# Performance work log

Measured on AMD Instinct MI355X. Metric: run time of the kernel, lower is better.

Reference implementation:

```python
import jax, jax.numpy as jnp
import numpy as np

B, N, C = 8, 4096, 1024
ATT_DIM = 512
M = 64  # num_outputs


def setup_inputs() -> dict:
    key = jax.random.key(0)
    k_x, k_w, k_b, k_av = jax.random.split(key, 4)
    x = jax.random.normal(k_x, (B, N, C), dtype=jnp.float32)
    # nn.Linear(input_dim, attention_dim): weight (att, C), bias (att,)
    lim = 1.0 / np.sqrt(C)
    W = jax.random.uniform(k_w, (ATT_DIM, C), dtype=jnp.float32, minval=-lim, maxval=lim)
    b = jax.random.uniform(k_b, (ATT_DIM,), dtype=jnp.float32, minval=-lim, maxval=lim)
    # torch.rand -> uniform [0,1)
    attention_vectors = jax.random.uniform(k_av, (M, ATT_DIM), dtype=jnp.float32)
    return {"x": x, "W": W, "b": b, "attention_vectors": attention_vectors}


def reference(x, W, b, attention_vectors):
    # linear projection: (B,N,C) @ (C,att) + bias -> (B,N,att)
    scores = jnp.einsum('bnc,dc->bnd', x, W) + b
    # learned-query attention logits: (B,M,N)
    logits = jnp.einsum('bnd,md->bmn', scores, attention_vectors)
    weights = jax.nn.softmax(logits, axis=-1)
    # pool original features: (B,M,N) @ (B,N,C) -> (B,M,C)
    return jnp.einsum('bmn,bnc->bmc', weights, x)
```

## Files before the change

### kernel.cpp

```cpp
#include <hip/hip_runtime.h>
#include <hip/hip_bf16.h>

#define Bn 8
#define Nn 4096
#define Cn 1024
#define Dn 512
#define Mn 64

typedef __hip_bfloat16 bf16;
typedef __attribute__((ext_vector_type(8))) short short8;
typedef __attribute__((ext_vector_type(4))) short short4x;
typedef __attribute__((ext_vector_type(4))) float f32x4;

#define MFMA16(a, b, c) __builtin_amdgcn_mfma_f32_16x16x32_bf16((a), (b), (c), 0, 0, 0)

__device__ inline short bfbits(float f) {
  union { bf16 b; short s; } u;
  u.b = __float2bfloat16(f);
  return u.s;
}

__device__ inline short8 pack8(const float4& a, const float4& b) {
  short8 s;
  s[0] = bfbits(a.x); s[1] = bfbits(a.y); s[2] = bfbits(a.z); s[3] = bfbits(a.w);
  s[4] = bfbits(b.x); s[5] = bfbits(b.y); s[6] = bfbits(b.z); s[7] = bfbits(b.w);
  return s;
}

__global__ __launch_bounds__(256) void prep_kernel(
    const float* __restrict__ W, const float* __restrict__ bias,
    const float* __restrict__ av, bf16* __restrict__ Vhi,
    bf16* __restrict__ Vlo, float* __restrict__ c0) {
  const int m = blockIdx.x;
  const int t = threadIdx.x;
  const int cl = t & 63, dg = t >> 6;
  const int c = blockIdx.y * 64 + cl;
  const float* wp = W + (size_t)(dg * 128) * Cn + c;
  const float* ap = av + m * Dn + dg * 128;
  float a0 = 0.f, a1 = 0.f, a2 = 0.f, a3 = 0.f;
#pragma unroll 8
  for (int i = 0; i < 128; i += 4) {
    a0 = fmaf(ap[i + 0], wp[(size_t)(i + 0) * Cn], a0);
    a1 = fmaf(ap[i + 1], wp[(size_t)(i + 1) * Cn], a1);
    a2 = fmaf(ap[i + 2], wp[(size_t)(i + 2) * Cn], a2);
    a3 = fmaf(ap[i + 3], wp[(size_t)(i + 3) * Cn], a3);
  }
  __shared__ float red[256];
  red[t] = (a0 + a1) + (a2 + a3);
  __syncthreads();
  const float v = red[cl] + red[cl + 64] + red[cl + 128] + red[cl + 192];
  if (dg == 0) {
    const bf16 hi = __float2bfloat16(v);
    Vhi[m * Cn + c] = hi;
    Vlo[m * Cn + c] = __float2bfloat16(v - __bfloat162float(hi));
  }
  if (blockIdx.y == 0) {
    __syncthreads();
    red[t] = av[m * Dn + t] * bias[t] + av[m * Dn + t + 256] * bias[t + 256];
    __syncthreads();
    if (t < 64) {
      float s = red[t] + red[t + 64] + red[t + 128] + red[t + 192];
#pragma unroll
      for (int off = 32; off > 0; off >>= 1) s += __shfl_down(s, off);
      if (t == 0) c0[m] = s;
    }
  }
}

__global__ __launch_bounds__(256) void logits_kernel(
    const float* __restrict__ x, const bf16* __restrict__ Vhi,
    const bf16* __restrict__ Vlo, const float* __restrict__ c0,
    float* __restrict__ logits) {
  const int n0 = blockIdx.x * 64;
  const int b = blockIdx.y;
  const int t = threadIdx.x;
  __shared__ short Vs[2][2][64][72];
  const int w = t >> 6, lane = t & 63, lr = lane & 15, q = lane >> 4;

  int vr[2], vc[2];
  const bf16 *hsrc[2], *lsrc[2];
#pragma unroll
  for (int j = 0; j < 2; ++j) {
    const int u = t + 256 * j;
    vr[j] = u >> 3;
    vc[j] = (u & 7) * 8;
    hsrc[j] = Vhi + vr[j] * Cn + vc[j];
    lsrc[j] = Vlo + vr[j] * Cn + vc[j];
  }
  const float* xrow = x + (size_t)(b * Nn + n0 + w * 16 + lr) * Cn + q * 8;

  f32x4 acc[4];
#pragma unroll
  for (int i = 0; i < 4; ++i) acc[i] = (f32x4){0.f, 0.f, 0.f, 0.f};

  short8 vh[2], vl[2];
  float4 xs0, xs1, xs2, xs3;

#pragma unroll
  for (int j = 0; j < 2; ++j) {
    vh[j] = *(const short8*)(hsrc[j]);
    vl[j] = *(const short8*)(lsrc[j]);
  }
  xs0 = *(const float4*)(xrow);
  xs1 = *(const float4*)(xrow + 4);
  xs2 = *(const float4*)(xrow + 32);
  xs3 = *(const float4*)(xrow + 36);
#pragma unroll
  for (int j = 0; j < 2; ++j) {
    *(short8*)&Vs[0][0][vr[j]][vc[j]] = vh[j];
    *(short8*)&Vs[0][1][vr[j]][vc[j]] = vl[j];
  }
#pragma unroll
  for (int j = 0; j < 2; ++j) {
    vh[j] = *(const short8*)(hsrc[j] + 64);
    vl[j] = *(const short8*)(lsrc[j] + 64);
  }
  __syncthreads();

#pragma unroll
  for (int kc = 0; kc < 16; ++kc) {
    const int buf = kc & 1;
    const short8 a0 = pack8(xs0, xs1);
    const short8 a1 = pack8(xs2, xs3);
    if (kc < 15) {
      const int k1 = (kc + 1) * 64;
      xs0 = *(const float4*)(xrow + k1);
      xs1 = *(const float4*)(xrow + k1 + 4);
      xs2 = *(const float4*)(xrow + k1 + 32);
      xs3 = *(const float4*)(xrow + k1 + 36);
    }
    if (kc < 15) {
#pragma unroll
      for (int j = 0; j < 2; ++j) {
        *(short8*)&Vs[buf ^ 1][0][vr[j]][vc[j]] = vh[j];
        *(short8*)&Vs[buf ^ 1][1][vr[j]][vc[j]] = vl[j];
      }
    }
    if (kc < 14) {
      const int k2 = (kc + 2) * 64;
#pragma unroll
      for (int j = 0; j < 2; ++j) {
        vh[j] = *(const short8*)(hsrc[j] + k2);
        vl[j] = *(const short8*)(lsrc[j] + k2);
      }
    }
#pragma unroll
    for (int kk2 = 0; kk2 < 2; ++kk2) {
      const short8 a = kk2 ? a1 : a0;
      const int ko = kk2 * 32 + q * 8;
#pragma unroll
      for (int mt = 0; mt < 4; ++mt) {
        acc[mt] = MFMA16(a, *(const short8*)&Vs[buf][0][mt * 16 + lr][ko], acc[mt]);
        acc[mt] = MFMA16(a, *(const short8*)&Vs[buf][1][mt * 16 + lr][ko], acc[mt]);
      }
    }
    __syncthreads();
  }

  float (*LT)[68] = reinterpret_cast<float(*)[68]>(&Vs[0][0][0][0]);
#pragma unroll
  for (int mt = 0; mt < 4; ++mt) {
    const int m = mt * 16 + lr;
    const float bb = c0[m];
    f32x4 o = acc[mt];
    o[0] += bb; o[1] += bb; o[2] += bb; o[3] += bb;
    *(f32x4*)&LT[m][w * 16 + q * 4] = o;
  }
  __syncthreads();
  {
    const int mr = t >> 2, seg = (t & 3) * 16;
    const float* srcL = &LT[mr][seg];
    float* dst = logits + (size_t)(b * Mn + mr) * Nn + n0 + seg;
#pragma unroll
    for (int i = 0; i < 4; ++i) *(float4*)(dst + 4 * i) = *(const float4*)(srcL + 4 * i);
  }
}

__global__ __launch_bounds__(256) void softmax_kernel(
    const float* __restrict__ logits, bf16* __restrict__ wgt) {
  const int row = blockIdx.x;
  const int t = threadIdx.x;
  const float* L = logits + (size_t)row * Nn;
  float v[16];
  float mx = -3.4e38f;
#pragma unroll
  for (int i = 0; i < 16; ++i) {
    v[i] = L[t + 256 * i];
    mx = fmaxf(mx, v[i]);
  }
#pragma unroll
  for (int off = 32; off > 0; off >>= 1) mx = fmaxf(mx, __shfl_down(mx, off));
  __shared__ float sred[4];
  if ((t & 63) == 0) sred[t >> 6] = mx;
  __syncthreads();
  mx = fmaxf(fmaxf(sred[0], sred[1]), fmaxf(sred[2], sred[3]));
  float sum = 0.f;
#pragma unroll
  for (int i = 0; i < 16; ++i) {
    v[i] = __expf(v[i] - mx);
    sum += v[i];
  }
#pragma unroll
  for (int off = 32; off > 0; off >>= 1) sum += __shfl_down(sum, off);
  __syncthreads();
  if ((t & 63) == 0) sred[t >> 6] = sum;
  __syncthreads();
  const float inv = 1.f / (sred[0] + sred[1] + sred[2] + sred[3]);
#pragma unroll
  for (int i = 0; i < 16; ++i)
    wgt[(size_t)row * Nn + t + 256 * i] = __float2bfloat16(v[i] * inv);
}

__global__ __launch_bounds__(256) void pool_kernel(
    const float* __restrict__ x, const bf16* __restrict__ wgt,
    float* __restrict__ part) {
  const int cbase = blockIdx.x * 64;
  const int b = blockIdx.y;
  const int ks = blockIdx.z;
  const int t = threadIdx.x;
  __shared__ short XT[2][64][72];
  const int w = t >> 6, lane = t & 63, lr = lane & 15, q = lane >> 4;
  const int mh = (w & 1) * 32, ch = (w >> 1) * 32;
  f32x4 acc[2][2];
#pragma unroll
  for (int i = 0; i < 2; ++i)
#pragma unroll
    for (int j = 0; j < 2; ++j) acc[i][j] = (f32x4){0.f, 0.f, 0.f, 0.f};

  const int h = t & 15, g = t >> 4;
  const int swz = 8 * (h & 7);
  const int swzr0 = 8 * (((ch + lr) >> 2) & 7);
  const int swzr1 = 8 * (((ch + 16 + lr) >> 2) & 7);
  const int kbase = ks * (Nn / 4);
  const float* xsrc = x + (size_t)b * Nn * Cn + (size_t)(kbase + 4 * g) * Cn + cbase + 4 * h;
  const bf16* wr0 = wgt + (size_t)(b * Mn + mh + lr) * Nn + kbase + q * 8;
  const bf16* wr1 = wr0 + (size_t)16 * Nn;

  float4 p0, p1, p2, p3;
  short8 aw0, aw1, aw2, aw3;

  p0 = *(const float4*)(xsrc);
  p1 = *(const float4*)(xsrc + Cn);
  p2 = *(const float4*)(xsrc + 2 * Cn);
  p3 = *(const float4*)(xsrc + 3 * Cn);
  aw0 = *(const short8*)(wr0);
  aw1 = *(const short8*)(wr0 + 32);
  aw2 = *(const short8*)(wr1);
  aw3 = *(const short8*)(wr1 + 32);
  {
    const int kof = (4 * g) ^ swz;
    short4x v0, v1, v2, v3;
    v0[0] = bfbits(p0.x); v0[1] = bfbits(p1.x); v0[2] = bfbits(p2.x); v0[3] = bfbits(p3.x);
    v1[0] = bfbits(p0.y); v1[1] = bfbits(p1.y); v1[2] = bfbits(p2.y); v1[3] = bfbits(p3.y);
    v2[0] = bfbits(p0.z); v2[1] = bfbits(p1.z); v2[2] = bfbits(p2.z); v2[3] = bfbits(p3.z);
    v3[0] = bfbits(p0.w); v3[1] = bfbits(p1.w); v3[2] = bfbits(p2.w); v3[3] = bfbits(p3.w);
    *(short4x*)&XT[0][4 * h + 0][kof] = v0;
    *(short4x*)&XT[0][4 * h + 1][kof] = v1;
    *(short4x*)&XT[0][4 * h + 2][kof] = v2;
    *(short4x*)&XT[0][4 * h + 3][kof] = v3;
  }
  p0 = *(const float4*)(xsrc + (size_t)64 * Cn);
  p1 = *(const float4*)(xsrc + (size_t)65 * Cn);
  p2 = *(const float4*)(xsrc + (size_t)66 * Cn);
  p3 = *(const float4*)(xsrc + (size_t)67 * Cn);
  __syncthreads();

#pragma unroll 4
  for (int kc = 0; kc < 16; ++kc) {
    const int buf = kc & 1;
    const short8 a00 = aw0, a01 = aw1, a10 = aw2, a11 = aw3;
    if (kc < 15) {
      const int k1 = (kc + 1) * 64;
      aw0 = *(const short8*)(wr0 + k1);
      aw1 = *(const short8*)(wr0 + k1 + 32);
      aw2 = *(const short8*)(wr1 + k1);
      aw3 = *(const short8*)(wr1 + k1 + 32);
    }
    if (kc < 15) {
      const int kof = (4 * g) ^ swz;
      short4x v0, v1, v2, v3;
      v0[0] = bfbits(p0.x); v0[1] = bfbits(p1.x); v0[2] = bfbits(p2.x); v0[3] = bfbits(p3.x);
      v1[0] = bfbits(p0.y); v1[1] = bfbits(p1.y); v1[2] = bfbits(p2.y); v1[3] = bfbits(p3.y);
      v2[0] = bfbits(p0.z); v2[1] = bfbits(p1.z); v2[2] = bfbits(p2.z); v2[3] = bfbits(p3.z);
      v3[0] = bfbits(p0.w); v3[1] = bfbits(p1.w); v3[2] = bfbits(p2.w); v3[3] = bfbits(p3.w);
      *(short4x*)&XT[buf ^ 1][4 * h + 0][kof] = v0;
      *(short4x*)&XT[buf ^ 1][4 * h + 1][kof] = v1;
      *(short4x*)&XT[buf ^ 1][4 * h + 2][kof] = v2;
      *(short4x*)&XT[buf ^ 1][4 * h + 3][kof] = v3;
    }
    if (kc < 14) {
      const size_t roff = (size_t)(kc + 2) * 64 * Cn;
      p0 = *(const float4*)(xsrc + roff);
      p1 = *(const float4*)(xsrc + roff + Cn);
      p2 = *(const float4*)(xsrc + roff + 2 * Cn);
      p3 = *(const float4*)(xsrc + roff + 3 * Cn);
    }
#pragma unroll
    for (int kk2 = 0; kk2 < 2; ++kk2) {
      const int ko = kk2 * 32 + q * 8;
      const short8 b0 = *(const short8*)&XT[buf][ch + lr][ko ^ swzr0];
      const short8 b1 = *(const short8*)&XT[buf][ch + 16 + lr][ko ^ swzr1];
      const short8 aa = kk2 ? a01 : a00;
      const short8 ab = kk2 ? a11 : a10;
      acc[0][0] = MFMA16(aa, b0, acc[0][0]);
      acc[0][1] = MFMA16(aa, b1, acc[0][1]);
      acc[1][0] = MFMA16(ab, b0, acc[1][0]);
      acc[1][1] = MFMA16(ab, b1, acc[1][1]);
    }
    __syncthreads();
  }

  float* pout = part + ((size_t)ks * Bn + b) * Mn * Cn;
#pragma unroll
  for (int mi = 0; mi < 2; ++mi)
#pragma unroll
    for (int ci = 0; ci < 2; ++ci) {
      const int m = mh + mi * 16 + q * 4;
      const int c = cbase + ch + ci * 16 + lr;
#pragma unroll
      for (int reg = 0; reg < 4; ++reg)
        pout[(size_t)(m + reg) * Cn + c] = acc[mi][ci][reg];
    }
}

__global__ __launch_bounds__(256) void reduce_kernel(
    const float* __restrict__ part, float* __restrict__ out) {
  const int i = blockIdx.x * 256 + threadIdx.x;
  const float4* p = (const float4*)part;
  const int S4 = (Bn * Mn * Cn) / 4;
  const float4 v0 = p[i], v1 = p[i + S4], v2 = p[i + 2 * S4], v3 = p[i + 3 * S4];
  float4 o;
  o.x = (v0.x + v1.x) + (v2.x + v3.x);
  o.y = (v0.y + v1.y) + (v2.y + v3.y);
  o.z = (v0.z + v1.z) + (v2.z + v3.z);
  o.w = (v0.w + v1.w) + (v2.w + v3.w);
  ((float4*)out)[i] = o;
}

extern "C" void kernel_launch(void* const* d_in, const int* in_sizes, int n_in,
                              void* d_out, int out_size, void* d_ws, size_t ws_size,
                              hipStream_t stream) {
  const float* x = (const float*)d_in[0];
  const float* W = (const float*)d_in[1];
  const float* bias = (const float*)d_in[2];
  const float* av = (const float*)d_in[3];
  float* out = (float*)d_out;
  char* ws = (char*)d_ws;

  bf16* Vhi = (bf16*)(ws + 0);
  bf16* Vlo = (bf16*)(ws + 131072);
  float* c0 = (float*)(ws + 262144);
  float* logits = (float*)(ws + 263168);
  bf16* wgt = (bf16*)(ws + 8651776);
  float* part = (float*)(ws + 12846080);

  prep_kernel<<<dim3(Mn, Cn / 64), 256, 0, stream>>>(W, bias, av, Vhi, Vlo, c0);
  logits_kernel<<<dim3(Nn / 64, Bn), 256, 0, stream>>>(x, Vhi, Vlo, c0, logits);
  softmax_kernel<<<Bn * Mn, 256, 0, stream>>>(logits, wgt);
  pool_kernel<<<dim3(Cn / 64, Bn, 4), 256, 0, stream>>>(x, wgt, part);
  reduce_kernel<<<(Bn * Mn * Cn) / 1024, 256, 0, stream>>>(part, out);
}
```

Measured before the change: 253.8 us.

## Double block size in logits and pool kernels and deepen pool split-K

The logits kernel moves to 512-thread blocks in which each wave computes two of the four M tiles rather than all four. This halves per-wave accumulators, but each x row is now loaded and converted by two waves. The pool kernel covers 128 channels per block with 8 waves and splits N eight ways instead of four, so the reduce kernel now sums eight partial slices. The aim is more waves in flight and better latency hiding, at the cost of a partial buffer twice as large and more reduction traffic.

```diff
diff --git a/kernel.cpp b/kernel.cpp
--- a/kernel.cpp
+++ b/kernel.cpp
@@ -67,7 +67,7 @@
   }
 }
 
-__global__ __launch_bounds__(256) void logits_kernel(
+__global__ __launch_bounds__(512) void logits_kernel(
     const float* __restrict__ x, const bf16* __restrict__ Vhi,
     const bf16* __restrict__ Vlo, const float* __restrict__ c0,
     float* __restrict__ logits) {
@@ -76,45 +76,31 @@
   const int t = threadIdx.x;
   __shared__ short Vs[2][2][64][72];
   const int w = t >> 6, lane = t & 63, lr = lane & 15, q = lane >> 4;
-
-  int vr[2], vc[2];
-  const bf16 *hsrc[2], *lsrc[2];
-#pragma unroll
-  for (int j = 0; j < 2; ++j) {
-    const int u = t + 256 * j;
-    vr[j] = u >> 3;
-    vc[j] = (u & 7) * 8;
-    hsrc[j] = Vhi + vr[j] * Cn + vc[j];
-    lsrc[j] = Vlo + vr[j] * Cn + vc[j];
-  }
-  const float* xrow = x + (size_t)(b * Nn + n0 + w * 16 + lr) * Cn + q * 8;
-
-  f32x4 acc[4];
-#pragma unroll
-  for (int i = 0; i < 4; ++i) acc[i] = (f32x4){0.f, 0.f, 0.f, 0.f};
-
-  short8 vh[2], vl[2];
+  const int nq = w & 3;
+  const int mtb = (w >> 2) * 2;
+
+  const int vr = t >> 3, vc = (t & 7) * 8;
+  const bf16* hsrc = Vhi + vr * Cn + vc;
+  const bf16* lsrc = Vlo + vr * Cn + vc;
+  const float* xrow = x + (size_t)(b * Nn + n0 + nq * 16 + lr) * Cn + q * 8;
+
+  f32x4 acc[2];
+  acc[0] = (f32x4){0.f, 0.f, 0.f, 0.f};
+  acc[1] = (f32x4){0.f, 0.f, 0.f, 0.f};
+
+  short8 vh, vl;
   float4 xs0, xs1, xs2, xs3;
 
-#pragma unroll
-  for (int j = 0; j < 2; ++j) {
-    vh[j] = *(const short8*)(hsrc[j]);
-    vl[j] = *(const short8*)(lsrc[j]);
-  }
+  vh = *(const short8*)(hsrc);
+  vl = *(const short8*)(lsrc);
   xs0 = *(const float4*)(xrow);
   xs1 = *(const float4*)(xrow + 4);
   xs2 = *(const float4*)(xrow + 32);
   xs3 = *(const float4*)(xrow + 36);
-#pragma unroll
-  for (int j = 0; j < 2; ++j) {
-    *(short8*)&Vs[0][0][vr[j]][vc[j]] = vh[j];
-    *(short8*)&Vs[0][1][vr[j]][vc[j]] = vl[j];
-  }
-#pragma unroll
-  for (int j = 0; j < 2; ++j) {
-    vh[j] = *(const short8*)(hsrc[j] + 64);
-    vl[j] = *(const short8*)(lsrc[j] + 64);
-  }
+  *(short8*)&Vs[0][0][vr][vc] = vh;
+  *(short8*)&Vs[0][1][vr][vc] = vl;
+  vh = *(const short8*)(hsrc + 64);
+  vl = *(const short8*)(lsrc + 64);
   __syncthreads();
 
 #pragma unroll
@@ -130,28 +116,23 @@
       xs3 = *(const float4*)(xrow + k1 + 36);
     }
     if (kc < 15) {
-#pragma unroll
-      for (int j = 0; j < 2; ++j) {
-        *(short8*)&Vs[buf ^ 1][0][vr[j]][vc[j]] = vh[j];
-        *(short8*)&Vs[buf ^ 1][1][vr[j]][vc[j]] = vl[j];
-      }
+      *(short8*)&Vs[buf ^ 1][0][vr][vc] = vh;
+      *(short8*)&Vs[buf ^ 1][1][vr][vc] = vl;
     }
     if (kc < 14) {
       const int k2 = (kc + 2) * 64;
-#pragma unroll
-      for (int j = 0; j < 2; ++j) {
-        vh[j] = *(const short8*)(hsrc[j] + k2);
-        vl[j] = *(const short8*)(lsrc[j] + k2);
-      }
+      vh = *(const short8*)(hsrc + k2);
+      vl = *(const short8*)(lsrc + k2);
     }
 #pragma unroll
     for (int kk2 = 0; kk2 < 2; ++kk2) {
       const short8 a = kk2 ? a1 : a0;
       const int ko = kk2 * 32 + q * 8;
 #pragma unroll
-      for (int mt = 0; mt < 4; ++mt) {
-        acc[mt] = MFMA16(a, *(const short8*)&Vs[buf][0][mt * 16 + lr][ko], acc[mt]);
-        acc[mt] = MFMA16(a, *(const short8*)&Vs[buf][1][mt * 16 + lr][ko], acc[mt]);
+      for (int i = 0; i < 2; ++i) {
+        const int mt = mtb + i;
+        acc[i] = MFMA16(a, *(const short8*)&Vs[buf][0][mt * 16 + lr][ko], acc[i]);
+        acc[i] = MFMA16(a, *(const short8*)&Vs[buf][1][mt * 16 + lr][ko], acc[i]);
       }
     }
     __syncthreads();
@@ -159,20 +140,19 @@
 
   float (*LT)[68] = reinterpret_cast<float(*)[68]>(&Vs[0][0][0][0]);
 #pragma unroll
-  for (int mt = 0; mt < 4; ++mt) {
-    const int m = mt * 16 + lr;
+  for (int i = 0; i < 2; ++i) {
+    const int m = (mtb + i) * 16 + lr;
+    f32x4 o = acc[i];
     const float bb = c0[m];
-    f32x4 o = acc[mt];
     o[0] += bb; o[1] += bb; o[2] += bb; o[3] += bb;
-    *(f32x4*)&LT[m][w * 16 + q * 4] = o;
+    *(f32x4*)&LT[m][nq * 16 + q * 4] = o;
   }
   __syncthreads();
   {
-    const int mr = t >> 2, seg = (t & 3) * 16;
-    const float* srcL = &LT[mr][seg];
+    const int mr = t >> 3, seg = (t & 7) * 8;
     float* dst = logits + (size_t)(b * Mn + mr) * Nn + n0 + seg;
-#pragma unroll
-    for (int i = 0; i < 4; ++i) *(float4*)(dst + 4 * i) = *(const float4*)(srcL + 4 * i);
+    *(float4*)(dst) = *(const float4*)&LT[mr][seg];
+    *(float4*)(dst + 4) = *(const float4*)&LT[mr][seg + 4];
   }
 }
 
@@ -211,14 +191,14 @@
     wgt[(size_t)row * Nn + t + 256 * i] = __float2bfloat16(v[i] * inv);
 }
 
-__global__ __launch_bounds__(256) void pool_kernel(
+__global__ __launch_bounds__(512) void pool_kernel(
     const float* __restrict__ x, const bf16* __restrict__ wgt,
     float* __restrict__ part) {
-  const int cbase = blockIdx.x * 64;
+  const int cbase = blockIdx.x * 128;
   const int b = blockIdx.y;
   const int ks = blockIdx.z;
   const int t = threadIdx.x;
-  __shared__ short XT[2][64][72];
+  __shared__ short XT[2][128][72];
   const int w = t >> 6, lane = t & 63, lr = lane & 15, q = lane >> 4;
   const int mh = (w & 1) * 32, ch = (w >> 1) * 32;
   f32x4 acc[2][2];
@@ -227,11 +207,11 @@
 #pragma unroll
     for (int j = 0; j < 2; ++j) acc[i][j] = (f32x4){0.f, 0.f, 0.f, 0.f};
 
-  const int h = t & 15, g = t >> 4;
+  const int h = t & 31, g = t >> 5;
   const int swz = 8 * (h & 7);
   const int swzr0 = 8 * (((ch + lr) >> 2) & 7);
   const int swzr1 = 8 * (((ch + 16 + lr) >> 2) & 7);
-  const int kbase = ks * (Nn / 4);
+  const int kbase = ks * (Nn / 8);
   const float* xsrc = x + (size_t)b * Nn * Cn + (size_t)(kbase + 4 * g) * Cn + cbase + 4 * h;
   const bf16* wr0 = wgt + (size_t)(b * Mn + mh + lr) * Nn + kbase + q * 8;
   const bf16* wr1 = wr0 + (size_t)16 * Nn;
@@ -265,18 +245,18 @@
   p3 = *(const float4*)(xsrc + (size_t)67 * Cn);
   __syncthreads();
 
-#pragma unroll 4
-  for (int kc = 0; kc < 16; ++kc) {
+#pragma unroll
+  for (int kc = 0; kc < 8; ++kc) {
     const int buf = kc & 1;
     const short8 a00 = aw0, a01 = aw1, a10 = aw2, a11 = aw3;
-    if (kc < 15) {
+    if (kc < 7) {
       const int k1 = (kc + 1) * 64;
       aw0 = *(const short8*)(wr0 + k1);
       aw1 = *(const short8*)(wr0 + k1 + 32);
       aw2 = *(const short8*)(wr1 + k1);
       aw3 = *(const short8*)(wr1 + k1 + 32);
     }
-    if (kc < 15) {
+    if (kc < 7) {
       const int kof = (4 * g) ^ swz;
       short4x v0, v1, v2, v3;
       v0[0] = bfbits(p0.x); v0[1] = bfbits(p1.x); v0[2] = bfbits(p2.x); v0[3] = bfbits(p3.x);
@@ -288,7 +268,7 @@
       *(short4x*)&XT[buf ^ 1][4 * h + 2][kof] = v2;
       *(short4x*)&XT[buf ^ 1][4 * h + 3][kof] = v3;
     }
-    if (kc < 14) {
+    if (kc < 6) {
       const size_t roff = (size_t)(kc + 2) * 64 * Cn;
       p0 = *(const float4*)(xsrc + roff);
       p1 = *(const float4*)(xsrc + roff + Cn);
@@ -328,12 +308,12 @@
   const int i = blockIdx.x * 256 + threadIdx.x;
   const float4* p = (const float4*)part;
   const int S4 = (Bn * Mn * Cn) / 4;
-  const float4 v0 = p[i], v1 = p[i + S4], v2 = p[i + 2 * S4], v3 = p[i + 3 * S4];
-  float4 o;
-  o.x = (v0.x + v1.x) + (v2.x + v3.x);
-  o.y = (v0.y + v1.y) + (v2.y + v3.y);
-  o.z = (v0.z + v1.z) + (v2.z + v3.z);
-  o.w = (v0.w + v1.w) + (v2.w + v3.w);
+  float4 o = p[i];
+#pragma unroll
+  for (int j = 1; j < 8; ++j) {
+    const float4 v = p[i + j * S4];
+    o.x += v.x; o.y += v.y; o.z += v.z; o.w += v.w;
+  }
   ((float4*)out)[i] = o;
 }
 
@@ -355,8 +335,8 @@
   float* part = (float*)(ws + 12846080);
 
   prep_kernel<<<dim3(Mn, Cn / 64), 256, 0, stream>>>(W, bias, av, Vhi, Vlo, c0);
-  logits_kernel<<<dim3(Nn / 64, Bn), 256, 0, stream>>>(x, Vhi, Vlo, c0, logits);
+  logits_kernel<<<dim3(Nn / 64, Bn), 512, 0, stream>>>(x, Vhi, Vlo, c0, logits);
   softmax_kernel<<<Bn * Mn, 256, 0, stream>>>(logits, wgt);
-  pool_kernel<<<dim3(Cn / 64, Bn, 4), 256, 0, stream>>>(x, wgt, part);
+  pool_kernel<<<dim3(Cn / 128, Bn, 8), 512, 0, stream>>>(x, wgt, part);
   reduce_kernel<<<(Bn * Mn * Cn) / 1024, 256, 0, stream>>>(part, out);
 }
```

Result: no change. 257.4 us (+1.4%).
